# Kernel optimization log

Measured on AMD Instinct MI355X. Metric: run time of the kernel, lower is better.

## Reference

```python
import jax, jax.numpy as jnp
import numpy as np
from jax import lax

K = 7          # local attention kernel size
DIL = 2        # dilation
PAD = 6        # padding -> same spatial size
BN_EPS = 1e-5


def setup_inputs() -> dict:
    key = jax.random.key(0)
    ks = jax.random.split(key, 4)
    B, C, H, W = 16, 256, 56, 56
    x = jax.random.normal(ks[0], (B, C, H, W), dtype=jnp.float32)
    # conv weights scaled for stable activations
    w1 = jax.random.normal(ks[1], (128, C, K, K), dtype=jnp.float32) * 0.02
    b1 = jnp.zeros((128,), dtype=jnp.float32)
    w2 = jax.random.normal(ks[2], (49, 128, 1, 1), dtype=jnp.float32) * 0.05
    b2 = jnp.zeros((49,), dtype=jnp.float32)
    gamma = jnp.ones((49,), dtype=jnp.float32)
    beta = jnp.zeros((49,), dtype=jnp.float32)
    running_mean = jnp.zeros((49,), dtype=jnp.float32)
    running_var = jnp.ones((49,), dtype=jnp.float32)
    return {"x": x, "w1": w1, "b1": b1, "w2": w2, "b2": b2,
            "gamma": gamma, "beta": beta,
            "running_mean": running_mean, "running_var": running_var}


def _picanet_l(x, w1, b1, w2, b2, gamma, beta, running_mean, running_var):
    B, C, H, W = x.shape
    # conv1: 7x7, dilation 2, padding 6 (same size)
    k = lax.conv_general_dilated(
        x, w1, window_strides=(1, 1), padding=((PAD, PAD), (PAD, PAD)),
        rhs_dilation=(DIL, DIL),
        dimension_numbers=("NCHW", "OIHW", "NCHW"))
    k = jax.nn.relu(k + b1[None, :, None, None])
    # conv2: 1x1 -> 49 channels
    k = jnp.einsum("bchw,oc->bohw", k, w2[:, :, 0, 0]) + b2[None, :, None, None]
    # BatchNorm (eval-style, running stats), then relu + softmax over the 49 taps
    inv = gamma * lax.rsqrt(running_var + BN_EPS)
    k = (k - running_mean[None, :, None, None]) * inv[None, :, None, None] + beta[None, :, None, None]
    k = jax.nn.relu(k)
    attn = jax.nn.softmax(k, axis=1)  # [B, 49, H, W]
    # unfold-gather + weighted sum, expressed as 49 shifted slices of the
    # zero-padded input (matches F.unfold(x, 7, dilation=2, padding=6)).
    xpad = jnp.pad(x, ((0, 0), (0, 0), (PAD, PAD), (PAD, PAD)))
    out = jnp.zeros_like(x)
    for i in range(K):
        for j in range(K):
            tap = xpad[:, :, DIL * i: DIL * i + H, DIL * j: DIL * j + W]  # [B,C,H,W]
            out = out + tap * attn[:, i * K + j][:, None]
    return out


def reference(x, w1, b1, w2, b2, gamma, beta, running_mean, running_var):
    return _picanet_l(x, w1, b1, w2, b2, gamma, beta, running_mean, running_var)
```

## Files before the change

kernel.cpp:

```cpp
#include <hip/hip_runtime.h>

typedef _Float16 f16;
typedef __attribute__((__ext_vector_type__(4))) _Float16 f16x4;
typedef __attribute__((__ext_vector_type__(8))) _Float16 f16x8;
typedef __attribute__((__ext_vector_type__(4))) float f32x4;

#define GLDS16(g, l) __builtin_amdgcn_global_load_lds( \
    (const __attribute__((address_space(1))) void*)(g), \
    (__attribute__((address_space(3))) void*)(l), 16, 0, 0)


__global__ __launch_bounds__(256) void zero_border(uint4* __restrict__ xp) {
  const int i = blockIdx.x * 256 + threadIdx.x;
  int idx4;
  if (i < 417792) {
    int u = i % 2176;
    int row12 = i / 2176;
    int b = row12 / 12, r12 = row12 % 12;
    int r = (r12 < 6) ? r12 : r12 + 56;
    idx4 = (b * 68 + r) * 2176 + u;
  } else {
    int j = i - 417792;
    int u = j % 192;
    int run = j / 192;
    int side = run & 1;
    int br = run >> 1;
    int r = br % 56 + 6, b = br / 56;
    idx4 = (b * 68 + r) * 2176 + (side ? 62 * 32 : 0) + u;
  }
  xp[idx4] = make_uint4(0u, 0u, 0u, 0u);
}

__global__ __launch_bounds__(256) void transpose_cast(
    const float* __restrict__ x, f16* __restrict__ xpad) {
  __shared__ f16 t16[56][258];
  const int bh = blockIdx.x;
  const int h = bh % 56, b = bh / 56;
  const float* xp = x + (size_t)b * 256 * 3136 + h * 56;
  for (int f = threadIdx.x; f < 256 * 56; f += 256) {
    int c = f / 56, w = f % 56;
    t16[w][c] = (f16)xp[(size_t)c * 3136 + w];
  }
  __syncthreads();
  f16* op = xpad + (((size_t)(b * 68) + h + 6) * 68 + 6) * 256;
  for (int g = threadIdx.x; g < 56 * 32; g += 256) {
    int w = g >> 5, c0 = (g & 31) * 8;
    *(f16x8*)(op + (size_t)w * 256 + c0) = *(const f16x8*)&t16[w][c0];
  }
}

__global__ __launch_bounds__(256) void w1_transform(
    const float* __restrict__ w1, f16* __restrict__ w1h) {
  const int idx = blockIdx.x * 256 + threadIdx.x;
  const int co = idx >> 8, c = idx & 255;
  const int half = c >> 7, cc = (c >> 5) & 3, q = (c >> 3) & 3, e = c & 7;
  const int f = co >> 4, l15 = co & 15;
  const size_t base =
      ((((size_t)(half * 4 + cc) * 8 + f) * 64 + q * 16 + l15) * 8 + e);
  const float* src = w1 + ((size_t)co * 256 + c) * 49;
#pragma unroll 7
  for (int ij = 0; ij < 49; ++ij)
    w1h[base + (size_t)ij * 32768] = (f16)src[ij];
}

__global__ __launch_bounds__(256, 2) void conv1_gemm(
    const f16* __restrict__ xpad, const f16* __restrict__ w1h,
    f16* __restrict__ kbuf) {
  __shared__ f16 strip[16 * 68 * 32];

  const int tid = threadIdx.x;
  const int wid = tid >> 6, lane = tid & 63;
  const int pphys = blockIdx.x;
  const int bid = (pphys & 7) * 56 + (pphys >> 3);
  const int half = bid & 1;
  const int sid = bid >> 1;
  const int b = sid / 14;
  const int h0 = (sid % 14) * 4;

  const int l15 = lane & 15;
  const int q = lane >> 4;
  const int qb = (l15 >> 1) & 3;

  const int mbase = (wid >> 1) * 7;
  const int nbase = (wid & 1) * 4;

  int arow_off[7];
#pragma unroll
  for (int mm = 0; mm < 7; ++mm) {
    int p = (mbase + mm) * 16 + l15;
    int rw = p / 56;
    int w = p - 56 * rw;
    arow_off[mm] = (rw * 68 + w) * 64;
  }

  const char* xg = (const char*)xpad +
                   ((size_t)(b * 68 + h0)) * (68 * 512) + half * 256;
  const char* wB = (const char*)w1h;
  char* Ss = (char*)strip;

  const int half4 = half * 4;
  auto loadB = [&](int cc, int ij, int nn) -> f16x8 {
    int off = (((ij * 8 + half4 + cc) * 8 + nbase + nn) * 64 + lane) * 16;
    return *(const f16x8*)(wB + off);
  };

  f32x4 acc[7][4] = {};
  f16x8 c0 = loadB(0, 0, 0), c1 = loadB(0, 0, 1);
  f16x8 c2 = loadB(0, 0, 2), c3 = loadB(0, 0, 3);
  f16x8 n0 = loadB(0, 1, 0), n1 = loadB(0, 1, 1);
  f16x8 n2 = loadB(0, 1, 2), n3 = loadB(0, 1, 3);
  int lcc = 0, lij = 2;

  for (int cc = 0; cc < 4; ++cc) {
    const int chb = cc * 64;
    __syncthreads();
#pragma unroll
    for (int rr = 0; rr < 17; ++rr) {
      int s = rr * 256 + tid;
      int r = (int)((unsigned)s / 272u);
      int rem = s - r * 272;
      int col = rem >> 2, q4 = rem & 3;
      int qq = q4 ^ ((col >> 1) & 3);
      GLDS16(xg + (size_t)r * (68 * 512) + col * 512 + chb + qq * 16,
             Ss + (rr * 256 + wid * 64) * 16);
    }
    __syncthreads();

#pragma unroll 7
    for (int ij = 0; ij < 49; ++ij) {
      f16x8 u0 = c0, u1 = c1, u2 = c2, u3 = c3;
      c0 = n0; c1 = n1; c2 = n2; c3 = n3;
      if (lcc < 4) {
        n0 = loadB(lcc, lij, 0);
        n1 = loadB(lcc, lij, 1);
        n2 = loadB(lcc, lij, 2);
        n3 = loadB(lcc, lij, 3);
        if (++lij == 49) { lij = 0; ++lcc; }
      }
      const int i = (int)((unsigned)ij / 7u);
      const int j = ij - 7 * i;
      const int base_off = i * 8704 + j * 128 + ((q ^ ((qb + j) & 3)) << 4);
      __builtin_amdgcn_s_setprio(1);
#pragma unroll
      for (int mm = 0; mm < 7; ++mm) {
        f16x8 a = *(const f16x8*)(Ss + arow_off[mm] + base_off);
        acc[mm][0] = __builtin_amdgcn_mfma_f32_16x16x32_f16(a, u0,
                                                            acc[mm][0], 0, 0, 0);
        acc[mm][1] = __builtin_amdgcn_mfma_f32_16x16x32_f16(a, u1,
                                                            acc[mm][1], 0, 0, 0);
        acc[mm][2] = __builtin_amdgcn_mfma_f32_16x16x32_f16(a, u2,
                                                            acc[mm][2], 0, 0, 0);
        acc[mm][3] = __builtin_amdgcn_mfma_f32_16x16x32_f16(a, u3,
                                                            acc[mm][3], 0, 0, 0);
      }
      __builtin_amdgcn_s_setprio(0);
    }
  }

  f16* kh = kbuf + (size_t)half * (50176 * 128);
  const int pbase = (b * 56 + h0) * 56;
#pragma unroll
  for (int mm = 0; mm < 7; ++mm) {
#pragma unroll
    for (int nn = 0; nn < 4; ++nn) {
      const int co = (nbase + nn) * 16 + l15;
#pragma unroll
      for (int r = 0; r < 4; ++r) {
        int p = (mbase + mm) * 16 + q * 4 + r;
        int rw = p / 56;
        int w = p - 56 * rw;
        kh[(size_t)(pbase + rw * 56 + w) * 128 + co] = (f16)acc[mm][nn][r];
      }
    }
  }
}

__global__ __launch_bounds__(128) void conv2_bn_softmax(
    const f16* __restrict__ kbuf, const float* __restrict__ b1,
    const float* __restrict__ w2, const float* __restrict__ b2,
    const float* __restrict__ gamma, const float* __restrict__ beta,
    const float* __restrict__ rmean, const float* __restrict__ rvar,
    float* __restrict__ attn) {
  __shared__ float w2s[49 * 128];
  __shared__ float b1s[128];
  __shared__ float outs[128 * 49];
  for (int i = threadIdx.x; i < 49 * 128; i += 128) w2s[i] = w2[i];
  if (threadIdx.x < 128) b1s[threadIdx.x] = b1[threadIdx.x];
  __syncthreads();
  const int p = blockIdx.x * 128 + threadIdx.x;
  float acc[49];
#pragma unroll
  for (int o = 0; o < 49; ++o) acc[o] = 0.f;
  const f16x8* ka = (const f16x8*)(kbuf + (size_t)p * 128);
  const f16x8* kb = (const f16x8*)(kbuf + (size_t)50176 * 128 + (size_t)p * 128);
  for (int u = 0; u < 16; ++u) {
    f16x8 va = ka[u], vb = kb[u];
    float kv[8];
#pragma unroll
    for (int j = 0; j < 8; ++j) {
      float s = (float)va[j] + (float)vb[j] + b1s[u * 8 + j];
      kv[j] = s > 0.f ? s : 0.f;
    }
#pragma unroll
    for (int o = 0; o < 49; ++o) {
      const float* wrow = w2s + o * 128 + u * 8;
#pragma unroll
      for (int j = 0; j < 8; ++j) acc[o] = fmaf(kv[j], wrow[j], acc[o]);
    }
  }
  float mx = -1e30f;
#pragma unroll
  for (int o = 0; o < 49; ++o) {
    float s = acc[o] + b2[o];
    float inv = gamma[o] * rsqrtf(rvar[o] + 1e-5f);
    s = (s - rmean[o]) * inv + beta[o];
    s = s > 0.f ? s : 0.f;
    acc[o] = s;
    mx = fmaxf(mx, s);
  }
  float sum = 0.f;
#pragma unroll
  for (int o = 0; o < 49; ++o) {
    float e = __expf(acc[o] - mx);
    acc[o] = e;
    sum += e;
  }
  const float rinv = 1.f / sum;
  float* orow = outs + threadIdx.x * 49;
#pragma unroll
  for (int o = 0; o < 49; ++o) orow[o] = acc[o] * rinv;
  __syncthreads();
  float* ab = attn + (size_t)blockIdx.x * (128 * 49);
  for (int i = threadIdx.x; i < 128 * 49; i += 128) ab[i] = outs[i];
}

__global__ __launch_bounds__(896, 1) void aggregate2(
    const f16* __restrict__ xpad, const float* __restrict__ attn,
    float* __restrict__ out) {
  __shared__ float t[256][57];
  const int bh = blockIdx.x;
  const int h = bh % 56, b = bh / 56;
  const int tid = threadIdx.x;
  const int wid = tid >> 6, lane = tid & 63;
  const int q = (wid < 7) ? wid * 8 : (wid - 7) * 8 + 1;

  int ap[4];
#pragma unroll
  for (int p = 0; p < 4; ++p) ap[p] = ((b * 56 + h) * 56 + q + 2 * p) * 49;

  float acc[4][4] = {};
  const f16* rowb = xpad + ((size_t)(b * 68 + h) * 68 + q) * 256 + 4 * lane;

  for (int i = 0; i < 7; ++i) {
    const f16* rb = rowb + (size_t)(2 * i * 68) * 256;
#pragma unroll
    for (int tt = 0; tt < 10; ++tt) {
      f16x4 xv = *(const f16x4*)(rb + tt * 512);
      float xf[4];
#pragma unroll
      for (int k = 0; k < 4; ++k) xf[k] = (float)xv[k];
#pragma unroll
      for (int p = 0; p < 4; ++p) {
        const int j = tt - p;
        if (j >= 0 && j < 7) {
          const float a = attn[ap[p] + i * 7 + j];
#pragma unroll
          for (int k = 0; k < 4; ++k) acc[p][k] = fmaf(a, xf[k], acc[p][k]);
        }
      }
    }
  }

#pragma unroll
  for (int p = 0; p < 4; ++p)
#pragma unroll
    for (int k = 0; k < 4; ++k) t[4 * lane + k][q + 2 * p] = acc[p][k];
  __syncthreads();
  float* ob = out + ((size_t)b * 256 * 56 + h) * 56;
  for (int f = tid; f < 256 * 56; f += 896) {
    int c = f / 56, w = f % 56;
    ob[(size_t)c * 3136 + w] = t[c][w];
  }
}

extern "C" void kernel_launch(void* const* d_in, const int* in_sizes, int n_in,
                              void* d_out, int out_size, void* d_ws,
                              size_t ws_size, hipStream_t stream) {
  const float* x = (const float*)d_in[0];
  const float* w1 = (const float*)d_in[1];
  const float* b1 = (const float*)d_in[2];
  const float* w2 = (const float*)d_in[3];
  const float* b2 = (const float*)d_in[4];
  const float* gamma = (const float*)d_in[5];
  const float* beta = (const float*)d_in[6];
  const float* rmean = (const float*)d_in[7];
  const float* rvar = (const float*)d_in[8];
  float* out = (float*)d_out;

  char* ws = (char*)d_ws;
  f16* xpad = (f16*)ws;
  f16* w1h = (f16*)(ws + 37879808);
  f16* kbuf = (f16*)(ws + 41091072);
  float* attn = (float*)(ws + 66781184);

  hipLaunchKernelGGL(zero_border, dim3(2976), dim3(256), 0, stream,
                     (uint4*)xpad);
  hipLaunchKernelGGL(transpose_cast, dim3(896), dim3(256), 0, stream, x, xpad);
  hipLaunchKernelGGL(w1_transform, dim3(128), dim3(256), 0, stream, w1, w1h);
  hipLaunchKernelGGL(conv1_gemm, dim3(448), dim3(256), 0, stream, xpad, w1h,
                     kbuf);
  hipLaunchKernelGGL(conv2_bn_softmax, dim3(392), dim3(128), 0, stream, kbuf,
                     b1, w2, b2, gamma, beta, rmean, rvar, attn);
  hipLaunchKernelGGL(aggregate2, dim3(896), dim3(896), 0, stream, xpad, attn,
                     out);
}
```

Before: 296.6 us.

## Fuse prep kernels, restructure conv1 B/A prefetch, use fdot2 in conv2, remap aggregate blocks

Merges the border-zero, transpose-cast and weight-transform kernels into one launch to cut launch overhead and the gaps between launches. In conv1 it swaps the two-stage B register prefetch for a single-stage one, software-pipelines the LDS A-fragment loads across the mm loop, and drops the s_setprio hints. conv2 keeps w2 in LDS as f16 and uses packed fdot2, which halves LDS traffic but lowers the precision of the products. aggregate2 gets an XCD-aware block remap meant to improve cache locality.

New measurement: 257.3 us. 1.15x faster.

```diff
diff --git a/kernel.cpp b/kernel.cpp
--- a/kernel.cpp
+++ b/kernel.cpp
@@ -1,6 +1,7 @@
 #include <hip/hip_runtime.h>
 
 typedef _Float16 f16;
+typedef __attribute__((__ext_vector_type__(2))) _Float16 f16x2;
 typedef __attribute__((__ext_vector_type__(4))) _Float16 f16x4;
 typedef __attribute__((__ext_vector_type__(8))) _Float16 f16x8;
 typedef __attribute__((__ext_vector_type__(4))) float f32x4;
@@ -10,57 +11,57 @@
     (__attribute__((address_space(3))) void*)(l), 16, 0, 0)
 
 
-__global__ __launch_bounds__(256) void zero_border(uint4* __restrict__ xp) {
-  const int i = blockIdx.x * 256 + threadIdx.x;
-  int idx4;
-  if (i < 417792) {
-    int u = i % 2176;
-    int row12 = i / 2176;
-    int b = row12 / 12, r12 = row12 % 12;
-    int r = (r12 < 6) ? r12 : r12 + 56;
-    idx4 = (b * 68 + r) * 2176 + u;
+__global__ __launch_bounds__(256) void prep(
+    const float* __restrict__ x, const float* __restrict__ w1,
+    f16* __restrict__ xpad, f16* __restrict__ w1h) {
+  const int blk = blockIdx.x;
+  const int tid = threadIdx.x;
+  if (blk < 896) {
+    __shared__ f16 t16[56][258];
+    const int h = blk % 56, b = blk / 56;
+    const float* xp = x + (size_t)b * 256 * 3136 + h * 56;
+    for (int f = tid; f < 256 * 56; f += 256) {
+      int c = f / 56, w = f % 56;
+      t16[w][c] = (f16)xp[(size_t)c * 3136 + w];
+    }
+    __syncthreads();
+    f16* op = xpad + (((size_t)(b * 68) + h + 6) * 68 + 6) * 256;
+    for (int g = tid; g < 56 * 32; g += 256) {
+      int w = g >> 5, c0 = (g & 31) * 8;
+      *(f16x8*)(op + (size_t)w * 256 + c0) = *(const f16x8*)&t16[w][c0];
+    }
+  } else if (blk < 896 + 2976) {
+    const int i = (blk - 896) * 256 + tid;
+    uint4* xp4 = (uint4*)xpad;
+    int idx4;
+    if (i < 417792) {
+      int u = i % 2176;
+      int row12 = i / 2176;
+      int b = row12 / 12, r12 = row12 % 12;
+      int r = (r12 < 6) ? r12 : r12 + 56;
+      idx4 = (b * 68 + r) * 2176 + u;
+    } else {
+      int j = i - 417792;
+      int u = j % 192;
+      int run = j / 192;
+      int side = run & 1;
+      int br = run >> 1;
+      int r = br % 56 + 6, b = br / 56;
+      idx4 = (b * 68 + r) * 2176 + (side ? 62 * 32 : 0) + u;
+    }
+    xp4[idx4] = make_uint4(0u, 0u, 0u, 0u);
   } else {
-    int j = i - 417792;
-    int u = j % 192;
-    int run = j / 192;
-    int side = run & 1;
-    int br = run >> 1;
-    int r = br % 56 + 6, b = br / 56;
-    idx4 = (b * 68 + r) * 2176 + (side ? 62 * 32 : 0) + u;
-  }
-  xp[idx4] = make_uint4(0u, 0u, 0u, 0u);
-}
-
-__global__ __launch_bounds__(256) void transpose_cast(
-    const float* __restrict__ x, f16* __restrict__ xpad) {
-  __shared__ f16 t16[56][258];
-  const int bh = blockIdx.x;
-  const int h = bh % 56, b = bh / 56;
-  const float* xp = x + (size_t)b * 256 * 3136 + h * 56;
-  for (int f = threadIdx.x; f < 256 * 56; f += 256) {
-    int c = f / 56, w = f % 56;
-    t16[w][c] = (f16)xp[(size_t)c * 3136 + w];
-  }
-  __syncthreads();
-  f16* op = xpad + (((size_t)(b * 68) + h + 6) * 68 + 6) * 256;
-  for (int g = threadIdx.x; g < 56 * 32; g += 256) {
-    int w = g >> 5, c0 = (g & 31) * 8;
-    *(f16x8*)(op + (size_t)w * 256 + c0) = *(const f16x8*)&t16[w][c0];
-  }
-}
-
-__global__ __launch_bounds__(256) void w1_transform(
-    const float* __restrict__ w1, f16* __restrict__ w1h) {
-  const int idx = blockIdx.x * 256 + threadIdx.x;
-  const int co = idx >> 8, c = idx & 255;
-  const int half = c >> 7, cc = (c >> 5) & 3, q = (c >> 3) & 3, e = c & 7;
-  const int f = co >> 4, l15 = co & 15;
-  const size_t base =
-      ((((size_t)(half * 4 + cc) * 8 + f) * 64 + q * 16 + l15) * 8 + e);
-  const float* src = w1 + ((size_t)co * 256 + c) * 49;
+    const int idx = (blk - 3872) * 256 + tid;
+    const int co = idx >> 8, c = idx & 255;
+    const int half = c >> 7, cc = (c >> 5) & 3, q = (c >> 3) & 3, e = c & 7;
+    const int f = co >> 4, l15 = co & 15;
+    const size_t base =
+        ((((size_t)(half * 4 + cc) * 8 + f) * 64 + q * 16 + l15) * 8 + e);
+    const float* src = w1 + ((size_t)co * 256 + c) * 49;
 #pragma unroll 7
-  for (int ij = 0; ij < 49; ++ij)
-    w1h[base + (size_t)ij * 32768] = (f16)src[ij];
+    for (int ij = 0; ij < 49; ++ij)
+      w1h[base + (size_t)ij * 32768] = (f16)src[ij];
+  }
 }
 
 __global__ __launch_bounds__(256, 2) void conv1_gemm(
@@ -105,11 +106,8 @@
   };
 
   f32x4 acc[7][4] = {};
-  f16x8 c0 = loadB(0, 0, 0), c1 = loadB(0, 0, 1);
-  f16x8 c2 = loadB(0, 0, 2), c3 = loadB(0, 0, 3);
-  f16x8 n0 = loadB(0, 1, 0), n1 = loadB(0, 1, 1);
-  f16x8 n2 = loadB(0, 1, 2), n3 = loadB(0, 1, 3);
-  int lcc = 0, lij = 2;
+  f16x8 pb0 = loadB(0, 0, 0), pb1 = loadB(0, 0, 1);
+  f16x8 pb2 = loadB(0, 0, 2), pb3 = loadB(0, 0, 3);
 
   for (int cc = 0; cc < 4; ++cc) {
     const int chb = cc * 64;
@@ -128,32 +126,33 @@
 
 #pragma unroll 7
     for (int ij = 0; ij < 49; ++ij) {
-      f16x8 u0 = c0, u1 = c1, u2 = c2, u3 = c3;
-      c0 = n0; c1 = n1; c2 = n2; c3 = n3;
-      if (lcc < 4) {
-        n0 = loadB(lcc, lij, 0);
-        n1 = loadB(lcc, lij, 1);
-        n2 = loadB(lcc, lij, 2);
-        n3 = loadB(lcc, lij, 3);
-        if (++lij == 49) { lij = 0; ++lcc; }
+      f16x8 b0 = pb0, b1 = pb1, b2 = pb2, b3 = pb3;
+      int nij = ij + 1, ncc = cc;
+      if (nij == 49) { nij = 0; ++ncc; }
+      if (ncc < 4) {
+        pb0 = loadB(ncc, nij, 0);
+        pb1 = loadB(ncc, nij, 1);
+        pb2 = loadB(ncc, nij, 2);
+        pb3 = loadB(ncc, nij, 3);
       }
       const int i = (int)((unsigned)ij / 7u);
       const int j = ij - 7 * i;
       const int base_off = i * 8704 + j * 128 + ((q ^ ((qb + j) & 3)) << 4);
-      __builtin_amdgcn_s_setprio(1);
+      f16x8 a0 = *(const f16x8*)(Ss + arow_off[0] + base_off);
 #pragma unroll
       for (int mm = 0; mm < 7; ++mm) {
-        f16x8 a = *(const f16x8*)(Ss + arow_off[mm] + base_off);
-        acc[mm][0] = __builtin_amdgcn_mfma_f32_16x16x32_f16(a, u0,
+        f16x8 an = a0;
+        if (mm < 6) an = *(const f16x8*)(Ss + arow_off[mm + 1] + base_off);
+        acc[mm][0] = __builtin_amdgcn_mfma_f32_16x16x32_f16(a0, b0,
                                                             acc[mm][0], 0, 0, 0);
-        acc[mm][1] = __builtin_amdgcn_mfma_f32_16x16x32_f16(a, u1,
+        acc[mm][1] = __builtin_amdgcn_mfma_f32_16x16x32_f16(a0, b1,
                                                             acc[mm][1], 0, 0, 0);
-        acc[mm][2] = __builtin_amdgcn_mfma_f32_16x16x32_f16(a, u2,
+        acc[mm][2] = __builtin_amdgcn_mfma_f32_16x16x32_f16(a0, b2,
                                                             acc[mm][2], 0, 0, 0);
-        acc[mm][3] = __builtin_amdgcn_mfma_f32_16x16x32_f16(a, u3,
+        acc[mm][3] = __builtin_amdgcn_mfma_f32_16x16x32_f16(a0, b3,
                                                             acc[mm][3], 0, 0, 0);
+        a0 = an;
       }
-      __builtin_amdgcn_s_setprio(0);
     }
   }
 
@@ -181,10 +180,10 @@
     const float* __restrict__ gamma, const float* __restrict__ beta,
     const float* __restrict__ rmean, const float* __restrict__ rvar,
     float* __restrict__ attn) {
-  __shared__ float w2s[49 * 128];
+  __shared__ f16 w2s[49 * 128];
   __shared__ float b1s[128];
   __shared__ float outs[128 * 49];
-  for (int i = threadIdx.x; i < 49 * 128; i += 128) w2s[i] = w2[i];
+  for (int i = threadIdx.x; i < 49 * 128; i += 128) w2s[i] = (f16)w2[i];
   if (threadIdx.x < 128) b1s[threadIdx.x] = b1[threadIdx.x];
   __syncthreads();
   const int p = blockIdx.x * 128 + threadIdx.x;
@@ -195,17 +194,30 @@
   const f16x8* kb = (const f16x8*)(kbuf + (size_t)50176 * 128 + (size_t)p * 128);
   for (int u = 0; u < 16; ++u) {
     f16x8 va = ka[u], vb = kb[u];
-    float kv[8];
-#pragma unroll
-    for (int j = 0; j < 8; ++j) {
-      float s = (float)va[j] + (float)vb[j] + b1s[u * 8 + j];
-      kv[j] = s > 0.f ? s : 0.f;
+    f16x2 kvh[4];
+#pragma unroll
+    for (int j = 0; j < 4; ++j) {
+      float s0 = (float)va[2 * j] + (float)vb[2 * j] + b1s[u * 8 + 2 * j];
+      float s1 =
+          (float)va[2 * j + 1] + (float)vb[2 * j + 1] + b1s[u * 8 + 2 * j + 1];
+      s0 = s0 > 0.f ? s0 : 0.f;
+      s1 = s1 > 0.f ? s1 : 0.f;
+      kvh[j] = f16x2{(f16)s0, (f16)s1};
     }
 #pragma unroll
     for (int o = 0; o < 49; ++o) {
-      const float* wrow = w2s + o * 128 + u * 8;
-#pragma unroll
-      for (int j = 0; j < 8; ++j) acc[o] = fmaf(kv[j], wrow[j], acc[o]);
+      f16x8 wv = *(const f16x8*)(w2s + o * 128 + u * 8);
+#if __has_builtin(__builtin_amdgcn_fdot2)
+      acc[o] = __builtin_amdgcn_fdot2(kvh[0], f16x2{wv[0], wv[1]}, acc[o], false);
+      acc[o] = __builtin_amdgcn_fdot2(kvh[1], f16x2{wv[2], wv[3]}, acc[o], false);
+      acc[o] = __builtin_amdgcn_fdot2(kvh[2], f16x2{wv[4], wv[5]}, acc[o], false);
+      acc[o] = __builtin_amdgcn_fdot2(kvh[3], f16x2{wv[6], wv[7]}, acc[o], false);
+#else
+#pragma unroll
+      for (int j = 0; j < 4; ++j)
+        acc[o] += (float)kvh[j][0] * (float)wv[2 * j] +
+                  (float)kvh[j][1] * (float)wv[2 * j + 1];
+#endif
     }
   }
   float mx = -1e30f;
@@ -238,7 +250,8 @@
     const f16* __restrict__ xpad, const float* __restrict__ attn,
     float* __restrict__ out) {
   __shared__ float t[256][57];
-  const int bh = blockIdx.x;
+  const int pp = blockIdx.x;
+  const int bh = (pp & 7) * 112 + (pp >> 3);
   const int h = bh % 56, b = bh / 56;
   const int tid = threadIdx.x;
   const int wid = tid >> 6, lane = tid & 63;
@@ -303,10 +316,7 @@
   f16* kbuf = (f16*)(ws + 41091072);
   float* attn = (float*)(ws + 66781184);
 
-  hipLaunchKernelGGL(zero_border, dim3(2976), dim3(256), 0, stream,
-                     (uint4*)xpad);
-  hipLaunchKernelGGL(transpose_cast, dim3(896), dim3(256), 0, stream, x, xpad);
-  hipLaunchKernelGGL(w1_transform, dim3(128), dim3(256), 0, stream, w1, w1h);
+  hipLaunchKernelGGL(prep, dim3(4000), dim3(256), 0, stream, x, w1, xpad, w1h);
   hipLaunchKernelGGL(conv1_gemm, dim3(448), dim3(256), 0, stream, xpad, w1h,
                      kbuf);
   hipLaunchKernelGGL(conv2_bn_softmax, dim3(392), dim3(128), 0, stream, kbuf,
```
